# Optimization experiments

Measured on AMD Instinct MI355X. Metric: run time of the kernel, lower is better.

## Reference

```python
import jax, jax.numpy as jnp
import numpy as np

HEADS = 8
DIM_HEAD = 64


def setup_inputs() -> dict:
    key = jax.random.key(0)
    k1, k2, k3 = jax.random.split(key, 3)
    dim = 512
    hidden = HEADS * DIM_HEAD  # 512
    x = jax.random.normal(k1, (16, dim, 64, 64), dtype=jnp.float32)
    # 1x1 convs are matmuls over channels; store weights as [out_ch, in_ch]
    w_qkv = jax.random.normal(k2, (3 * hidden, dim), dtype=jnp.float32) * (1.0 / np.sqrt(dim))
    w_out = jax.random.normal(k3, (dim, hidden), dtype=jnp.float32) * (1.0 / np.sqrt(hidden))
    b_out = jnp.zeros((dim,), dtype=jnp.float32)
    return {"x": x, "w_qkv": w_qkv, "w_out": w_out, "b_out": b_out}


def reference(x, w_qkv, w_out, b_out):
    b, c, h, w = x.shape
    n = h * w
    xf = x.reshape(b, c, n)                          # [b, c, n]
    qkv = jnp.einsum('oc,bcn->bon', w_qkv, xf)        # 1x1 conv, no bias -> [b, 3*H*D, n]
    qkv = qkv.reshape(b, 3, HEADS, DIM_HEAD, n)       # split (qkv heads c)
    q, k, v = qkv[:, 0], qkv[:, 1], qkv[:, 2]         # each [b, H, D, n]
    k = jax.nn.softmax(k, axis=-1)                    # softmax over spatial tokens
    context = jnp.einsum('bhdn,bhen->bhde', k, v)     # [b, H, D, D]
    out = jnp.einsum('bhde,bhdn->bhen', context, q)   # [b, H, D, n]
    out = out.reshape(b, HEADS * DIM_HEAD, n)
    out = jnp.einsum('oc,bcn->bon', w_out, out) + b_out[None, :, None]  # 1x1 conv + bias
    return out.reshape(b, -1, h, w)
```

## Files before the change

kernel.cpp:

```cpp
#include <hip/hip_runtime.h>
#include <hip/hip_bf16.h>
#include <math.h>


typedef __attribute__((ext_vector_type(8))) __bf16 bf16x8;
typedef __attribute__((ext_vector_type(4))) float f32x4;

__device__ inline void async_ld16(const void* g, void* s) {
    __builtin_amdgcn_global_load_lds(
        (const __attribute__((address_space(1))) void*)g,
        (__attribute__((address_space(3))) void*)s, 16, 0, 0);
}

template<bool OUTBF, bool BIAS>
__global__ __launch_bounds__(256) void gemm_mfma(
    const __bf16* __restrict__ A, const __bf16* __restrict__ BT,
    void* __restrict__ Cv, const float* __restrict__ bias,
    int K, int N, long aBS, long bBS, long cBS)
{
    __shared__ __bf16 As[128 * 64];
    __shared__ __bf16 Bs[128 * 64];

    const int t = threadIdx.x;
    const int lane = t & 63, wv = t >> 6;
    const int z = blockIdx.z;

    const int nx = gridDim.x, ny = gridDim.y;
    const int orig = blockIdx.y * nx + blockIdx.x;
    const int cpx = (nx * ny) >> 3;
    const int w = (orig & 7) * cpx + (orig >> 3);
    const int bx = w / ny, by = w % ny;
    const int row0 = by * 128, col0 = bx * 128;

    A  += (long)z * aBS;
    BT += (long)z * bBS;

    const int wm = (wv >> 1) * 64, wn = (wv & 1) * 64;
    const int lr = lane & 15, kg = lane >> 4;

    f32x4 acc[4][4] = {};

    const int srow = t >> 3;
    const int gsrc = (t & 7) ^ ((t >> 3) & 7);
    const int swzR = lr & 7;

    for (int k0 = 0; k0 < K; k0 += 64) {
        #pragma unroll
        for (int rnd = 0; rnd < 4; rnd++) {
            int r = rnd * 32 + srow;
            async_ld16(A  + (long)(row0 + r) * K + k0 + gsrc * 8, &As[rnd * 2048 + t * 8]);
            async_ld16(BT + (long)(col0 + r) * K + k0 + gsrc * 8, &Bs[rnd * 2048 + t * 8]);
        }
        __syncthreads();

        #pragma unroll
        for (int kk = 0; kk < 2; kk++) {
            bf16x8 af[4], bfr[4];
            int ga = ((kk << 2) | kg) ^ swzR;
            #pragma unroll
            for (int i = 0; i < 4; i++) {
                af[i]  = *(const bf16x8*)&As[(wm + i * 16 + lr) * 64 + ga * 8];
                bfr[i] = *(const bf16x8*)&Bs[(wn + i * 16 + lr) * 64 + ga * 8];
            }
            #pragma unroll
            for (int i = 0; i < 4; i++)
                #pragma unroll
                for (int j = 0; j < 4; j++)
                    acc[i][j] = __builtin_amdgcn_mfma_f32_16x16x32_bf16(af[i], bfr[j], acc[i][j], 0, 0, 0);
        }
        __syncthreads();
    }

    #pragma unroll
    for (int i = 0; i < 4; i++) {
        #pragma unroll
        for (int j = 0; j < 4; j++) {
            #pragma unroll
            for (int r = 0; r < 4; r++) {
                int row = row0 + wm + i * 16 + kg * 4 + r;
                int col = col0 + wn + j * 16 + lr;
                float v = acc[i][j][r];
                if (OUTBF) {
                    ((__hip_bfloat16*)Cv)[(long)z * cBS + (long)row * N + col] = __float2bfloat16(v);
                } else {
                    if (BIAS) v += bias[row];
                    ((float*)Cv)[(long)z * cBS + (long)row * N + col] = v;
                }
            }
        }
    }
}

__global__ __launch_bounds__(256) void transpose_cast(
    const float* __restrict__ x, __hip_bfloat16* __restrict__ xT)
{
    __shared__ float tile[32][33];
    int z = blockIdx.z;
    int n0 = blockIdx.x * 32, c0 = blockIdx.y * 32;
    int tx = threadIdx.x & 31, ty = threadIdx.x >> 5;

    const float* xb = x + (long)z * 512 * 4096;
    #pragma unroll
    for (int i = 0; i < 4; i++)
        tile[ty + i * 8][tx] = xb[(long)(c0 + ty + i * 8) * 4096 + n0 + tx];
    __syncthreads();

    __hip_bfloat16* xTb = xT + (long)z * 4096 * 512;
    #pragma unroll
    for (int i = 0; i < 4; i++) {
        int nl = ty + i * 8;
        xTb[(long)(n0 + nl) * 512 + c0 + tx] = __float2bfloat16(tile[tx][nl]);
    }
}

__global__ __launch_bounds__(256) void transpose_cast_sq(
    const float* __restrict__ in, __hip_bfloat16* __restrict__ out)
{
    __shared__ float tile[32][33];
    int r0 = blockIdx.y * 32, c0 = blockIdx.x * 32;
    int tx = threadIdx.x & 31, ty = threadIdx.x >> 5;
    #pragma unroll
    for (int i = 0; i < 4; i++)
        tile[ty + i * 8][tx] = in[(long)(r0 + ty + i * 8) * 512 + c0 + tx];
    __syncthreads();
    #pragma unroll
    for (int i = 0; i < 4; i++)
        out[(long)(c0 + ty + i * 8) * 512 + r0 + tx] = __float2bfloat16(tile[tx][ty + i * 8]);
}

__global__ __launch_bounds__(256) void cast_bf(
    const float* __restrict__ in, __hip_bfloat16* __restrict__ out, int n)
{
    for (int i = blockIdx.x * 256 + threadIdx.x; i < n; i += gridDim.x * 256)
        out[i] = __float2bfloat16(in[i]);
}

__global__ __launch_bounds__(256) void row_stats(
    const __hip_bfloat16* __restrict__ kv, float2* __restrict__ stats)
{
    int b = blockIdx.x >> 9;
    int r = blockIdx.x & 511;
    const unsigned short* row = (const unsigned short*)(kv + ((long)b * 1024 + r) * 4096);

    int t = threadIdx.x, lane = t & 63, wv = t >> 6;
    __shared__ float red[8];

    float vals[16];
    float m = -INFINITY;
    #pragma unroll
    for (int i = 0; i < 2; i++) {
        uint4 raw = *(const uint4*)&row[8 * t + 2048 * i];
        unsigned v[4] = {raw.x, raw.y, raw.z, raw.w};
        #pragma unroll
        for (int j = 0; j < 4; j++) {
            float lo = __uint_as_float(v[j] << 16);
            float hi = __uint_as_float(v[j] & 0xffff0000u);
            vals[i * 8 + j * 2]     = lo;
            vals[i * 8 + j * 2 + 1] = hi;
            m = fmaxf(m, fmaxf(lo, hi));
        }
    }
    #pragma unroll
    for (int off = 32; off > 0; off >>= 1) m = fmaxf(m, __shfl_down(m, off));
    if (lane == 0) red[wv] = m;
    __syncthreads();
    if (t == 0) red[0] = fmaxf(fmaxf(red[0], red[1]), fmaxf(red[2], red[3]));
    __syncthreads();
    m = red[0];

    float s = 0.0f;
    #pragma unroll
    for (int i = 0; i < 16; i++) s += __expf(vals[i] - m);
    #pragma unroll
    for (int off = 32; off > 0; off >>= 1) s += __shfl_down(s, off);
    if (lane == 0) red[4 + wv] = s;
    __syncthreads();
    if (t == 0) {
        float stot = red[4] + red[5] + red[6] + red[7];
        stats[blockIdx.x] = make_float2(m, 1.0f / stot);
    }
}

__global__ __launch_bounds__(256) void ctx_mfma(
    const __hip_bfloat16* __restrict__ kv, const float2* __restrict__ stats,
    float* __restrict__ part)
{
    int ks = blockIdx.x, bh = blockIdx.y;
    int b = bh >> 3, h = bh & 7;
    const __hip_bfloat16* Krow = kv + ((long)b * 1024 + h * 64) * 4096 + ks * 512;
    const __hip_bfloat16* Vrow = kv + ((long)b * 1024 + 512 + h * 64) * 4096 + ks * 512;

    __shared__ __bf16 Ps[64 * 32];
    __shared__ __bf16 Vs[64 * 32];

    int t = threadIdx.x, lane = t & 63, wv = t >> 6;
    int lr = lane & 15, kg = lane >> 4;

    int prow = t >> 2, pc = (t & 3) * 8;
    float2 s2 = stats[b * 512 + h * 64 + prow];
    float pm = s2.x, pinv = s2.y;

    f32x4 acc[4] = {};

    for (int k0 = 0; k0 < 512; k0 += 32) {
        {
            int vrow = wv * 16 + (lane >> 2);
            int vc   = (lane & 3) * 8;
            async_ld16(Vrow + (long)vrow * 4096 + k0 + vc, &Vs[wv * 16 * 32 + lane * 8]);
        }
        {
            uint4 raw = *(const uint4*)(Krow + (long)prow * 4096 + k0 + pc);
            unsigned v[4] = {raw.x, raw.y, raw.z, raw.w};
            __hip_bfloat16 pb[8];
            #pragma unroll
            for (int j = 0; j < 4; j++) {
                float lo = __uint_as_float(v[j] << 16);
                float hi = __uint_as_float(v[j] & 0xffff0000u);
                pb[j * 2]     = __float2bfloat16(__expf(lo - pm) * pinv);
                pb[j * 2 + 1] = __float2bfloat16(__expf(hi - pm) * pinv);
            }
            *(bf16x8*)&Ps[prow * 32 + pc] = *(const bf16x8*)pb;
        }
        __syncthreads();

        bf16x8 af = *(const bf16x8*)&Ps[(wv * 16 + lr) * 32 + kg * 8];
        #pragma unroll
        for (int j = 0; j < 4; j++) {
            bf16x8 bfr = *(const bf16x8*)&Vs[(j * 16 + lr) * 32 + kg * 8];
            acc[j] = __builtin_amdgcn_mfma_f32_16x16x32_bf16(af, bfr, acc[j], 0, 0, 0);
        }
        __syncthreads();
    }

    float* P = part + ((long)bh * 8 + ks) * 4096;
    #pragma unroll
    for (int j = 0; j < 4; j++)
        #pragma unroll
        for (int r = 0; r < 4; r++)
            P[(wv * 16 + kg * 4 + r) * 64 + j * 16 + lr] = acc[j][r];
}

__global__ __launch_bounds__(256) void reduce_ctx(
    const float* __restrict__ part, float* __restrict__ ctx)
{
    int bh = blockIdx.x;
    for (int i = threadIdx.x; i < 4096; i += 256) {
        float s = 0.0f;
        #pragma unroll
        for (int ks = 0; ks < 8; ks++)
            s += part[((long)bh * 8 + ks) * 4096 + i];
        ctx[(long)bh * 4096 + i] = s;
    }
}

__global__ __launch_bounds__(256) void gemm64_w2(
    const float* __restrict__ A, const float* __restrict__ Bm,
    __hip_bfloat16* __restrict__ Cb)
{
    const int t  = threadIdx.x;
    const int tx = t & 15;
    const int ty = t >> 4;
    const int z  = blockIdx.z;

    int row0 = blockIdx.y * 64;

    long aBase = (long)(z & 7) * 64;
    long bBase = (long)z * 4096;
    long cBase = (long)(z >> 3) * 262144 + (long)(z & 7) * 64;

    __shared__ __align__(16) float As[16][68];
    __shared__ __align__(16) float Bs[16][68];

    float acc[4][4] = {};

    for (int k0 = 0; k0 < 64; k0 += 16) {
        {
            int k = t & 15, r = t >> 4;
            #pragma unroll
            for (int i = 0; i < 4; i++)
                As[k][r + i * 16] = A[aBase + (long)(row0 + r + i * 16) * 512 + k0 + k];
        }
        {
            int k = t & 15, c = t >> 4;
            #pragma unroll
            for (int i = 0; i < 4; i++)
                Bs[k][c + i * 16] = Bm[bBase + (long)(c + i * 16) * 64 + k0 + k];
        }
        __syncthreads();

        #pragma unroll
        for (int kk = 0; kk < 16; kk++) {
            float4 a4 = *(const float4*)&As[kk][ty * 4];
            float4 b4 = *(const float4*)&Bs[kk][tx * 4];
            float av[4] = {a4.x, a4.y, a4.z, a4.w};
            float bv[4] = {b4.x, b4.y, b4.z, b4.w};
            #pragma unroll
            for (int i = 0; i < 4; i++)
                #pragma unroll
                for (int j = 0; j < 4; j++)
                    acc[i][j] = fmaf(av[i], bv[j], acc[i][j]);
        }
        __syncthreads();
    }

    #pragma unroll
    for (int i = 0; i < 4; i++) {
        int r = row0 + ty * 4 + i;
        __hip_bfloat16 o4[4];
        #pragma unroll
        for (int j = 0; j < 4; j++) o4[j] = __float2bfloat16(acc[i][j]);
        *(short4*)&Cb[cBase + (long)r * 512 + tx * 4] = *(const short4*)o4;
    }
}

extern "C" void kernel_launch(void* const* d_in, const int* in_sizes, int n_in,
                              void* d_out, int out_size, void* d_ws, size_t ws_size,
                              hipStream_t stream)
{
    const float* x     = (const float*)d_in[0];
    const float* w_qkv = (const float*)d_in[1];
    const float* w_out = (const float*)d_in[2];
    const float* b_out = (const float*)d_in[3];
    float* out = (float*)d_out;

    char* ws = (char*)d_ws;
    __hip_bfloat16* kv_bf  = (__hip_bfloat16*)(ws);
    __hip_bfloat16* xT     = (__hip_bfloat16*)(ws + 134217728L);
    float*          ctxp   = (float*)(ws + 201326592L);
    float*          ctx    = (float*)(ws + 218103808L);
    __hip_bfloat16* w2bf   = (__hip_bfloat16*)(ws + 220200960L);
    __hip_bfloat16* w3bf   = (__hip_bfloat16*)(ws + 228589568L);
    __hip_bfloat16* wkvbf  = (__hip_bfloat16*)(ws + 236978176L);
    __hip_bfloat16* wqT    = (__hip_bfloat16*)(ws + 238026752L);
    float2*         stats  = (float2*)(ws + 238551040L);

    transpose_cast<<<dim3(128, 16, 16), 256, 0, stream>>>(x, xT);
    cast_bf<<<dim3(512), 256, 0, stream>>>(w_qkv + 512 * 512, wkvbf, 1024 * 512);
    transpose_cast_sq<<<dim3(16, 16), 256, 0, stream>>>(w_qkv, wqT);

    gemm_mfma<true, false><<<dim3(32, 8, 16), 256, 0, stream>>>(
        (const __bf16*)wkvbf, (const __bf16*)xT, kv_bf, nullptr,
        512, 4096, 0L, (long)4096 * 512, (long)1024 * 4096);

    row_stats<<<dim3(8192), 256, 0, stream>>>(kv_bf, stats);

    ctx_mfma<<<dim3(8, 128), 256, 0, stream>>>(kv_bf, stats, ctxp);
    reduce_ctx<<<dim3(128), 256, 0, stream>>>(ctxp, ctx);

    gemm64_w2<<<dim3(1, 8, 128), 256, 0, stream>>>(w_out, ctx, w2bf);

    gemm_mfma<true, false><<<dim3(4, 4, 16), 256, 0, stream>>>(
        (const __bf16*)w2bf, (const __bf16*)wqT, w3bf, nullptr,
        512, 512, 262144L, 0L, 262144L);

    gemm_mfma<false, true><<<dim3(32, 4, 16), 256, 0, stream>>>(
        (const __bf16*)w3bf, (const __bf16*)xT, out, b_out,
        512, 4096, (long)512 * 512, (long)4096 * 512, (long)512 * 4096);
}
```

Baseline: 468.8 us.

## Add 256x256-tile GEMM with 4-stage async LDS pipeline for big GEMMs

Adds a new gemm256 kernel that uses 512 threads and 256x256 output tiles, with a 4-slot ring buffer of direct global-to-LDS async loads kept three K-tiles ahead. Split MFMA phases, explicit vmcnt waits, barriers and setprio are used to overlap loads with matrix math. The two large GEMMs (KV projection and final output projection) switch to it. Larger tiles increase data reuse and cut the grid size, but they also raise register and LDS pressure and leave fewer workgroups to spread across CUs.

```diff
diff --git a/kernel.cpp b/kernel.cpp
--- a/kernel.cpp
+++ b/kernel.cpp
@@ -10,6 +10,157 @@
     __builtin_amdgcn_global_load_lds(
         (const __attribute__((address_space(1))) void*)g,
         (__attribute__((address_space(3))) void*)s, 16, 0, 0);
+}
+
+template<int N> __device__ __forceinline__ void end_wait() {
+    if constexpr (N == 8)      asm volatile("s_waitcnt vmcnt(8)" ::: "memory");
+    else if constexpr (N == 4) asm volatile("s_waitcnt vmcnt(4)" ::: "memory");
+    else if constexpr (N == 0) asm volatile("s_waitcnt vmcnt(0)" ::: "memory");
+}
+
+template<bool STAGE, int ENDVM>
+__device__ __forceinline__ void tile_body(
+    __bf16* As, __bf16* Bs, int slot, int kt,
+    const __bf16* srcA0, const __bf16* srcA1,
+    const __bf16* srcB0, const __bf16* srcB1,
+    int dstA0, int dstA1, int dstB0, int dstB1,
+    int aBaseOff, int bBaseOff, f32x4 (&acc)[8][4])
+{
+    const int so = slot * 8192;
+    bf16x8 bfr[4], af[4];
+
+    #pragma unroll
+    for (int nf = 0; nf < 4; nf++)
+        bfr[nf] = *(const bf16x8*)&Bs[so + bBaseOff + nf * 128];
+    #pragma unroll
+    for (int mf = 0; mf < 4; mf++)
+        af[mf] = *(const bf16x8*)&As[so + aBaseOff + mf * 128];
+    if (STAGE) {
+        const int ns = (kt & 3) * 8192;
+        async_ld16(srcA0 + (long)kt * 32, &As[ns + dstA0]);
+        async_ld16(srcA1 + (long)kt * 32, &As[ns + dstA1]);
+    }
+    __builtin_amdgcn_s_barrier();
+    __builtin_amdgcn_s_setprio(1);
+    #pragma unroll
+    for (int mf = 0; mf < 4; mf++)
+        #pragma unroll
+        for (int nf = 0; nf < 4; nf++)
+            acc[mf][nf] = __builtin_amdgcn_mfma_f32_16x16x32_bf16(af[mf], bfr[nf], acc[mf][nf], 0, 0, 0);
+    __builtin_amdgcn_s_setprio(0);
+    __builtin_amdgcn_s_barrier();
+    __builtin_amdgcn_sched_barrier(0);
+
+    #pragma unroll
+    for (int mf = 0; mf < 4; mf++)
+        af[mf] = *(const bf16x8*)&As[so + aBaseOff + (4 + mf) * 128];
+    if (STAGE) {
+        const int ns = (kt & 3) * 8192;
+        async_ld16(srcB0 + (long)kt * 32, &Bs[ns + dstB0]);
+        async_ld16(srcB1 + (long)kt * 32, &Bs[ns + dstB1]);
+    }
+    __builtin_amdgcn_s_barrier();
+    __builtin_amdgcn_s_setprio(1);
+    #pragma unroll
+    for (int mf = 0; mf < 4; mf++)
+        #pragma unroll
+        for (int nf = 0; nf < 4; nf++)
+            acc[4 + mf][nf] = __builtin_amdgcn_mfma_f32_16x16x32_bf16(af[mf], bfr[nf], acc[4 + mf][nf], 0, 0, 0);
+    __builtin_amdgcn_s_setprio(0);
+    end_wait<ENDVM>();
+    __builtin_amdgcn_s_barrier();
+    __builtin_amdgcn_sched_barrier(0);
+}
+
+template<bool OUTBF, bool BIAS>
+__global__ __launch_bounds__(512, 2) void gemm256(
+    const __bf16* __restrict__ A, const __bf16* __restrict__ BT,
+    void* __restrict__ Cv, const float* __restrict__ bias,
+    int K, int N, long aBS, long bBS, long cBS)
+{
+    __shared__ __align__(16) __bf16 As[4 * 8192];
+    __shared__ __align__(16) __bf16 Bs[4 * 8192];
+
+    const int tid  = threadIdx.x;
+    const int lane = tid & 63, wv = tid >> 6;
+    const int lr = lane & 15, kg = lane >> 4;
+    const int wm = wv >> 2, wn = wv & 3;
+
+    const int gx = gridDim.x, gy = gridDim.y;
+    const unsigned nwg = gx * gy * gridDim.z;
+    const unsigned orig = (blockIdx.z * gy + blockIdx.y) * gx + blockIdx.x;
+    const unsigned q = nwg >> 3;
+    const unsigned w = (orig & 7) * q + (orig >> 3);
+    const unsigned perz = gx * gy;
+    const int z  = w / perz;
+    const unsigned rem = w - z * perz;
+    const int by = rem / gx, bx = rem - (rem / gx) * gx;
+    const int row0 = by * 256, col0 = bx * 256;
+
+    A  += (long)z * aBS;
+    BT += (long)z * bBS;
+
+    const int rowS = tid & 255;
+    const int gA0 = (tid >> 8);
+    const int gA1 = gA0 + 2;
+    const __bf16* srcA0 = A + (long)(row0 + rowS) * K + gA0 * 8;
+    const __bf16* srcA1 = A + (long)(row0 + rowS) * K + gA1 * 8;
+    const __bf16* srcB0 = BT + (long)(col0 + rowS) * K + gA0 * 8;
+    const __bf16* srcB1 = BT + (long)(col0 + rowS) * K + gA1 * 8;
+    const int dstA0 = gA0 * 2048 + rowS * 8;
+    const int dstA1 = gA1 * 2048 + rowS * 8;
+    const int dstB0 = dstA0;
+    const int dstB1 = dstA1;
+
+    const int aBaseOff = kg * 2048 + (wm * 128 + lr) * 8;
+    const int bBaseOff = kg * 2048 + (wn * 64 + lr) * 8;
+
+    f32x4 acc[8][4] = {};
+
+    const int nt = K >> 5;
+
+    #pragma unroll
+    for (int p = 0; p < 3; p++) {
+        const int ns = p * 8192;
+        async_ld16(srcA0 + p * 32, &As[ns + dstA0]);
+        async_ld16(srcA1 + p * 32, &As[ns + dstA1]);
+        async_ld16(srcB0 + p * 32, &Bs[ns + dstB0]);
+        async_ld16(srcB1 + p * 32, &Bs[ns + dstB1]);
+    }
+    asm volatile("s_waitcnt vmcnt(8)" ::: "memory");
+    __builtin_amdgcn_s_barrier();
+    __builtin_amdgcn_sched_barrier(0);
+
+    int t = 0;
+    for (; t < nt - 3; ++t)
+        tile_body<true, 8>(As, Bs, t & 3, t + 3, srcA0, srcA1, srcB0, srcB1,
+                           dstA0, dstA1, dstB0, dstB1, aBaseOff, bBaseOff, acc);
+    tile_body<false, 4>(As, Bs, t & 3, 0, srcA0, srcA1, srcB0, srcB1,
+                        dstA0, dstA1, dstB0, dstB1, aBaseOff, bBaseOff, acc); ++t;
+    tile_body<false, 0>(As, Bs, t & 3, 0, srcA0, srcA1, srcB0, srcB1,
+                        dstA0, dstA1, dstB0, dstB1, aBaseOff, bBaseOff, acc); ++t;
+    tile_body<false, -1>(As, Bs, t & 3, 0, srcA0, srcA1, srcB0, srcB1,
+                         dstA0, dstA1, dstB0, dstB1, aBaseOff, bBaseOff, acc);
+
+    const int kg4 = kg * 4;
+    #pragma unroll
+    for (int mf = 0; mf < 8; mf++) {
+        #pragma unroll
+        for (int nf = 0; nf < 4; nf++) {
+            #pragma unroll
+            for (int rr = 0; rr < 4; rr++) {
+                int row = row0 + wm * 128 + mf * 16 + kg4 + rr;
+                int col = col0 + wn * 64 + nf * 16 + lr;
+                float v = acc[mf][nf][rr];
+                if (OUTBF) {
+                    ((__hip_bfloat16*)Cv)[(long)z * cBS + (long)row * N + col] = __float2bfloat16(v);
+                } else {
+                    if (BIAS) v += bias[row];
+                    ((float*)Cv)[(long)z * cBS + (long)row * N + col] = v;
+                }
+            }
+        }
+    }
 }
 
 template<bool OUTBF, bool BIAS>
@@ -338,7 +489,7 @@
     cast_bf<<<dim3(512), 256, 0, stream>>>(w_qkv + 512 * 512, wkvbf, 1024 * 512);
     transpose_cast_sq<<<dim3(16, 16), 256, 0, stream>>>(w_qkv, wqT);
 
-    gemm_mfma<true, false><<<dim3(32, 8, 16), 256, 0, stream>>>(
+    gemm256<true, false><<<dim3(16, 4, 16), 512, 0, stream>>>(
         (const __bf16*)wkvbf, (const __bf16*)xT, kv_bf, nullptr,
         512, 4096, 0L, (long)4096 * 512, (long)1024 * 4096);
 
@@ -353,7 +504,7 @@
         (const __bf16*)w2bf, (const __bf16*)wqT, w3bf, nullptr,
         512, 512, 262144L, 0L, 262144L);
 
-    gemm_mfma<false, true><<<dim3(32, 4, 16), 256, 0, stream>>>(
+    gemm256<false, true><<<dim3(16, 2, 16), 512, 0, stream>>>(
         (const __bf16*)w3bf, (const __bf16*)xT, out, b_out,
         512, 4096, (long)512 * 512, (long)4096 * 512, (long)512 * 4096);
 }
```

New measurement: 523.0 us. +11.6%, slower.
